# Optimization experiments

Hardware: AMD Instinct MI355X
Metric: run time of the kernel (lower is better)

## Reference

```python
import jax, jax.numpy as jnp
import numpy as np

B = 1048576  # batch size
EPS_CLAMP_LO = 1e-6
EPS_CLAMP_HI = 1.0 - 1e-6


def _build_mask():
    # mask[k, i, j] = 1 iff i + j == k, flattened to [19, 100]
    i = np.arange(10)
    m = np.zeros((19, 10, 10), dtype=np.float32)
    ii, jj = np.meshgrid(i, i, indexing='ij')
    m[(ii + jj).ravel(), ii.ravel(), jj.ravel()] = 1.0
    return jnp.asarray(m.reshape(19, 100))


def setup_inputs() -> dict:
    key = jax.random.key(0)
    k1, k2, k3, k4 = jax.random.split(key, 4)
    # concept probabilities: uniform then normalize rows to sum 1
    p1 = jax.random.uniform(k1, (B, 10), dtype=jnp.float32)
    p1 = p1 / p1.sum(axis=1, keepdims=True)
    p2 = jax.random.uniform(k2, (B, 10), dtype=jnp.float32)
    p2 = p2 / p2.sum(axis=1, keepdims=True)
    # learnable permutation-tree weights (binaryTreeLogicNet leaf maps)
    W1 = jax.random.uniform(k3, (10, 10), dtype=jnp.float32)
    W2 = jax.random.uniform(k4, (10, 10), dtype=jnp.float32)
    mask = _build_mask()
    return {"p1": p1, "p2": p2, "W1": W1, "W2": W2, "mask": mask}


def _minmax_norm(W):
    lo = W.min(axis=1, keepdims=True)
    hi = W.max(axis=1, keepdims=True)
    return (W - lo) / (hi - lo + 1e-8)


def reference(p1, p2, W1, W2, mask):
    # input_to_leaf: learned soft permutation with minmax-normalized weights
    p1p = p1 @ _minmax_norm(W1)                      # [B,10]
    p2p = p2 @ _minmax_norm(W2)                      # [B,10]
    # MinMaxAggregator graded AND at andness=1.0 -> elementwise min over all pairs
    s = jnp.minimum(p1p[:, :, None], p2p[:, None, :])  # [B,10,10]
    one_minus = 1.0 - jnp.clip(s, EPS_CLAMP_LO, EPS_CLAMP_HI)
    log_one_minus = jnp.log(one_minus + 1e-12).reshape(-1, 100)  # [B,100]
    # fused masked reduction over all 19 sum bins: [B,100] @ [100,19]
    log_prod = log_one_minus @ mask.T                # [B,19]
    y_prob = 1.0 - jnp.exp(log_prod)                 # smooth OR per sum class
    y_prob = y_prob / (y_prob.sum(axis=1, keepdims=True) + 1e-9)
    return y_prob
```

## Files before the change

### kernel.cpp

```cpp
#include <hip/hip_runtime.h>


typedef float v2f __attribute__((ext_vector_type(2)));
typedef float v4f __attribute__((ext_vector_type(4)));

#define NBLOCKS 8192
#define TPB 64
#define ROWS 2

__global__ __launch_bounds__(TPB) void bacon_main(
    const float* __restrict__ p1, const float* __restrict__ p2,
    const float* __restrict__ W1, const float* __restrict__ W2,
    float* __restrict__ out)
{
    __shared__ __align__(16) float s_out[TPB * 19];
    __shared__ __align__(16) float s_w[240];

    const int t = threadIdx.x;
    const int blk = blockIdx.x;
    const size_t base = (size_t)blk * (TPB * ROWS);

    float2 va[ROWS][5], vb[ROWS][5];
    #pragma unroll
    for (int r = 0; r < ROWS; ++r) {
        const float2* g1 = (const float2*)(p1 + (base + (size_t)r * TPB + t) * 10);
        const float2* g2 = (const float2*)(p2 + (base + (size_t)r * TPB + t) * 10);
        #pragma unroll
        for (int e = 0; e < 5; ++e) { va[r][e] = g1[e]; vb[r][e] = g2[e]; }
    }

    if (t < 20) {
        const float* row = ((t < 10) ? W1 : W2) + (t % 10) * 10;
        float r[10];
        #pragma unroll
        for (int i = 0; i < 10; ++i) r[i] = row[i];
        float lo = r[0], hi = r[0];
        #pragma unroll
        for (int i = 1; i < 10; ++i) {
            lo = fminf(lo, r[i]);
            hi = fmaxf(hi, r[i]);
        }
        float inv = 1.0f / (hi - lo + 1e-8f);
        float* o = s_w + ((t < 10) ? 0 : 120) + (t % 10) * 12;
        #pragma unroll
        for (int i = 0; i < 10; ++i) o[i] = (r[i] - lo) * inv;
        o[10] = 0.0f; o[11] = 0.0f;
    }
    __syncthreads();

    float a[ROWS][10], b[ROWS][10];
    #pragma unroll
    for (int r = 0; r < ROWS; ++r)
        #pragma unroll
        for (int e = 0; e < 5; ++e) {
            a[r][2 * e] = va[r][e].x; a[r][2 * e + 1] = va[r][e].y;
            b[r][2 * e] = vb[r][e].x; b[r][2 * e + 1] = vb[r][e].y;
        }

    v2f A2[ROWS][5], B2[ROWS][5];
    #pragma unroll
    for (int r = 0; r < ROWS; ++r)
        #pragma unroll
        for (int m = 0; m < 5; ++m) { A2[r][m] = (v2f){1.0f, 1.0f}; B2[r][m] = (v2f){1.0f, 1.0f}; }

    #pragma unroll
    for (int k = 0; k < 10; ++k) {
        const float4* w1q = (const float4*)(s_w + k * 12);
        const float4* w2q = (const float4*)(s_w + 120 + k * 12);
        float4 u0 = w1q[0], u1 = w1q[1];
        float2 u2 = *(const float2*)(s_w + k * 12 + 8);
        float4 v0 = w2q[0], v1 = w2q[1];
        float2 v2 = *(const float2*)(s_w + 120 + k * 12 + 8);
        v2f uw[5] = { {u0.x, u0.y}, {u0.z, u0.w}, {u1.x, u1.y}, {u1.z, u1.w}, {u2.x, u2.y} };
        v2f vw[5] = { {v0.x, v0.y}, {v0.z, v0.w}, {v1.x, v1.y}, {v1.z, v1.w}, {v2.x, v2.y} };
        #pragma unroll
        for (int r = 0; r < ROWS; ++r) {
            const v2f na = (v2f){-a[r][k], -a[r][k]};
            const v2f nb = (v2f){-b[r][k], -b[r][k]};
            #pragma unroll
            for (int m = 0; m < 5; ++m) {
                A2[r][m] = __builtin_elementwise_fma(na, uw[m], A2[r][m]);
                B2[r][m] = __builtin_elementwise_fma(nb, vw[m], B2[r][m]);
            }
        }
    }

    #pragma unroll
    for (int r = 0; r < ROWS; ++r) {
        float A[10], Bv[10];
        #pragma unroll
        for (int m = 0; m < 5; ++m) {
            A[2 * m] = A2[r][m].x;  A[2 * m + 1] = A2[r][m].y;
            Bv[2 * m] = B2[r][m].x; Bv[2 * m + 1] = B2[r][m].y;
        }

        float prod[19];
        #pragma unroll
        for (int k = 0; k < 19; ++k) prod[k] = 1.0f;
        #pragma unroll
        for (int i = 0; i < 10; ++i) {
            #pragma unroll
            for (int j = 0; j < 10; ++j) {
                prod[i + j] *= fmaxf(A[i], Bv[j]);
            }
        }

        float y[19];
        float tot = 0.0f;
        #pragma unroll
        for (int k = 0; k < 19; ++k) { y[k] = 1.0f - prod[k]; tot += y[k]; }
        float invn = __builtin_amdgcn_rcpf(tot + 1e-9f);

        #pragma unroll
        for (int k = 0; k < 19; ++k) s_out[t * 19 + k] = y[k] * invn;
        __syncthreads();

        {
            const v4f* so = (const v4f*)s_out;
            v4f* go = (v4f*)(out + ((size_t)blk * ROWS + r) * (TPB * 19));
            #pragma unroll
            for (int it = 0; it < 5; ++it) {
                int idx = t + it * TPB;
                if (idx < 304)
                    __builtin_nontemporal_store(so[idx], go + idx);
            }
        }
    }
}

extern "C" void kernel_launch(void* const* d_in, const int* in_sizes, int n_in,
                              void* d_out, int out_size, void* d_ws, size_t ws_size,
                              hipStream_t stream) {
    const float* p1 = (const float*)d_in[0];
    const float* p2 = (const float*)d_in[1];
    const float* W1 = (const float*)d_in[2];
    const float* W2 = (const float*)d_in[3];
    bacon_main<<<NBLOCKS, TPB, 0, stream>>>(p1, p2, W1, W2, (float*)d_out);
}
```

Measured before the change: 153.9 us.

## Make blocks persistent over panels with async triple-buffered global-to-LDS loads

Each block now handles 8 panels of 128 rows instead of 128 rows total, cutting the grid from 8192 to 1024 blocks. Inputs are fetched with global_load_lds into three LDS slots, using manual vmcnt waits so loads for later panels overlap compute on the current one. The per-row __syncthreads before the output staging is dropped, which relies on the block being a single wavefront. The goal is to hide global load latency. In exchange the kernel runs far fewer waves per CU and uses more LDS per block.

```diff
diff --git a/kernel.cpp b/kernel.cpp
--- a/kernel.cpp
+++ b/kernel.cpp
@@ -3,31 +3,43 @@
 
 typedef float v2f __attribute__((ext_vector_type(2)));
 typedef float v4f __attribute__((ext_vector_type(4)));
+typedef __attribute__((address_space(3))) unsigned int lds_u32;
+typedef const __attribute__((address_space(1))) unsigned int g_u32;
 
-#define NBLOCKS 8192
+#define NBLOCKS 1024
 #define TPB 64
-#define ROWS 2
+#define PANELS 8
+#define PROWS 128
+#define SLOTS 3
 
 __global__ __launch_bounds__(TPB) void bacon_main(
     const float* __restrict__ p1, const float* __restrict__ p2,
     const float* __restrict__ W1, const float* __restrict__ W2,
     float* __restrict__ out)
 {
+    __shared__ __align__(16) float s_in[SLOTS][2560];
     __shared__ __align__(16) float s_out[TPB * 19];
     __shared__ __align__(16) float s_w[240];
 
     const int t = threadIdx.x;
     const int blk = blockIdx.x;
-    const size_t base = (size_t)blk * (TPB * ROWS);
+    const size_t blk_row0 = (size_t)blk * (PANELS * PROWS);
 
-    float2 va[ROWS][5], vb[ROWS][5];
-    #pragma unroll
-    for (int r = 0; r < ROWS; ++r) {
-        const float2* g1 = (const float2*)(p1 + (base + (size_t)r * TPB + t) * 10);
-        const float2* g2 = (const float2*)(p2 + (base + (size_t)r * TPB + t) * 10);
+    auto stage = [&](int p, int s) {
+        g_u32* gp1 = (g_u32*)(p1 + (blk_row0 + (size_t)p * PROWS) * 10);
+        g_u32* gp2 = (g_u32*)(p2 + (blk_row0 + (size_t)p * PROWS) * 10);
+        lds_u32* l1 = (lds_u32*)&s_in[s][0];
+        lds_u32* l2 = (lds_u32*)&s_in[s][1280];
         #pragma unroll
-        for (int e = 0; e < 5; ++e) { va[r][e] = g1[e]; vb[r][e] = g2[e]; }
-    }
+        for (int i = 0; i < 5; ++i) {
+            __builtin_amdgcn_global_load_lds(gp1 + i * 256 + t * 4, l1 + i * 256, 16, 0, 0);
+            __builtin_amdgcn_global_load_lds(gp2 + i * 256 + t * 4, l2 + i * 256, 16, 0, 0);
+        }
+    };
+
+    stage(0, 0);
+    stage(1, 1);
+    stage(2, 2);
 
     if (t < 20) {
         const float* row = ((t < 10) ? W1 : W2) + (t % 10) * 10;
@@ -48,81 +60,103 @@
     }
     __syncthreads();
 
-    float a[ROWS][10], b[ROWS][10];
     #pragma unroll
-    for (int r = 0; r < ROWS; ++r)
+    for (int p = 0; p < PANELS; ++p) {
+        const int s = p % SLOTS;
+
+        if (p <= PANELS - SLOTS) {
+            asm volatile("s_waitcnt vmcnt(20)" ::: "memory");
+        } else if (p == PANELS - 2) {
+            asm volatile("s_waitcnt vmcnt(10)" ::: "memory");
+        } else {
+            asm volatile("s_waitcnt vmcnt(0)" ::: "memory");
+        }
+        __builtin_amdgcn_sched_barrier(0);
+
+        float a[2][10], b[2][10];
         #pragma unroll
-        for (int e = 0; e < 5; ++e) {
-            a[r][2 * e] = va[r][e].x; a[r][2 * e + 1] = va[r][e].y;
-            b[r][2 * e] = vb[r][e].x; b[r][2 * e + 1] = vb[r][e].y;
-        }
-
-    v2f A2[ROWS][5], B2[ROWS][5];
-    #pragma unroll
-    for (int r = 0; r < ROWS; ++r)
-        #pragma unroll
-        for (int m = 0; m < 5; ++m) { A2[r][m] = (v2f){1.0f, 1.0f}; B2[r][m] = (v2f){1.0f, 1.0f}; }
-
-    #pragma unroll
-    for (int k = 0; k < 10; ++k) {
-        const float4* w1q = (const float4*)(s_w + k * 12);
-        const float4* w2q = (const float4*)(s_w + 120 + k * 12);
-        float4 u0 = w1q[0], u1 = w1q[1];
-        float2 u2 = *(const float2*)(s_w + k * 12 + 8);
-        float4 v0 = w2q[0], v1 = w2q[1];
-        float2 v2 = *(const float2*)(s_w + 120 + k * 12 + 8);
-        v2f uw[5] = { {u0.x, u0.y}, {u0.z, u0.w}, {u1.x, u1.y}, {u1.z, u1.w}, {u2.x, u2.y} };
-        v2f vw[5] = { {v0.x, v0.y}, {v0.z, v0.w}, {v1.x, v1.y}, {v1.z, v1.w}, {v2.x, v2.y} };
-        #pragma unroll
-        for (int r = 0; r < ROWS; ++r) {
-            const v2f na = (v2f){-a[r][k], -a[r][k]};
-            const v2f nb = (v2f){-b[r][k], -b[r][k]};
+        for (int rr = 0; rr < 2; ++rr) {
+            const int row = rr * 64 + t;
+            const v2f* r1 = (const v2f*)&s_in[s][row * 10];
+            const v2f* r2 = (const v2f*)&s_in[s][1280 + row * 10];
             #pragma unroll
-            for (int m = 0; m < 5; ++m) {
-                A2[r][m] = __builtin_elementwise_fma(na, uw[m], A2[r][m]);
-                B2[r][m] = __builtin_elementwise_fma(nb, vw[m], B2[r][m]);
+            for (int e = 0; e < 5; ++e) {
+                v2f x = r1[e], y = r2[e];
+                a[rr][2 * e] = x.x; a[rr][2 * e + 1] = x.y;
+                b[rr][2 * e] = y.x; b[rr][2 * e + 1] = y.y;
             }
         }
-    }
+        asm volatile("s_waitcnt lgkmcnt(0)" ::: "memory");
+        __builtin_amdgcn_sched_barrier(0);
 
-    #pragma unroll
-    for (int r = 0; r < ROWS; ++r) {
-        float A[10], Bv[10];
+        if (p + SLOTS < PANELS) stage(p + SLOTS, s);
+
+        v2f A2[2][5], B2[2][5];
         #pragma unroll
-        for (int m = 0; m < 5; ++m) {
-            A[2 * m] = A2[r][m].x;  A[2 * m + 1] = A2[r][m].y;
-            Bv[2 * m] = B2[r][m].x; Bv[2 * m + 1] = B2[r][m].y;
-        }
+        for (int rr = 0; rr < 2; ++rr)
+            #pragma unroll
+            for (int m = 0; m < 5; ++m) { A2[rr][m] = (v2f){1.0f, 1.0f}; B2[rr][m] = (v2f){1.0f, 1.0f}; }
 
-        float prod[19];
         #pragma unroll
-        for (int k = 0; k < 19; ++k) prod[k] = 1.0f;
-        #pragma unroll
-        for (int i = 0; i < 10; ++i) {
+        for (int k = 0; k < 10; ++k) {
+            const float4* w1q = (const float4*)(s_w + k * 12);
+            const float4* w2q = (const float4*)(s_w + 120 + k * 12);
+            float4 u0 = w1q[0], u1 = w1q[1];
+            float2 u2 = *(const float2*)(s_w + k * 12 + 8);
+            float4 v0 = w2q[0], v1 = w2q[1];
+            float2 v2 = *(const float2*)(s_w + 120 + k * 12 + 8);
+            v2f uw[5] = { {u0.x, u0.y}, {u0.z, u0.w}, {u1.x, u1.y}, {u1.z, u1.w}, {u2.x, u2.y} };
+            v2f vw[5] = { {v0.x, v0.y}, {v0.z, v0.w}, {v1.x, v1.y}, {v1.z, v1.w}, {v2.x, v2.y} };
             #pragma unroll
-            for (int j = 0; j < 10; ++j) {
-                prod[i + j] *= fmaxf(A[i], Bv[j]);
+            for (int rr = 0; rr < 2; ++rr) {
+                const v2f na = (v2f){-a[rr][k], -a[rr][k]};
+                const v2f nb = (v2f){-b[rr][k], -b[rr][k]};
+                #pragma unroll
+                for (int m = 0; m < 5; ++m) {
+                    A2[rr][m] = __builtin_elementwise_fma(na, uw[m], A2[rr][m]);
+                    B2[rr][m] = __builtin_elementwise_fma(nb, vw[m], B2[rr][m]);
+                }
             }
         }
 
-        float y[19];
-        float tot = 0.0f;
         #pragma unroll
-        for (int k = 0; k < 19; ++k) { y[k] = 1.0f - prod[k]; tot += y[k]; }
-        float invn = __builtin_amdgcn_rcpf(tot + 1e-9f);
+        for (int rr = 0; rr < 2; ++rr) {
+            float A[10], Bv[10];
+            #pragma unroll
+            for (int m = 0; m < 5; ++m) {
+                A[2 * m] = A2[rr][m].x;  A[2 * m + 1] = A2[rr][m].y;
+                Bv[2 * m] = B2[rr][m].x; Bv[2 * m + 1] = B2[rr][m].y;
+            }
 
-        #pragma unroll
-        for (int k = 0; k < 19; ++k) s_out[t * 19 + k] = y[k] * invn;
-        __syncthreads();
+            float prod[19];
+            #pragma unroll
+            for (int k = 0; k < 19; ++k) prod[k] = 1.0f;
+            #pragma unroll
+            for (int i = 0; i < 10; ++i) {
+                #pragma unroll
+                for (int j = 0; j < 10; ++j) {
+                    prod[i + j] *= fmaxf(A[i], Bv[j]);
+                }
+            }
 
-        {
-            const v4f* so = (const v4f*)s_out;
-            v4f* go = (v4f*)(out + ((size_t)blk * ROWS + r) * (TPB * 19));
+            float y[19];
+            float tot = 0.0f;
             #pragma unroll
-            for (int it = 0; it < 5; ++it) {
-                int idx = t + it * TPB;
-                if (idx < 304)
-                    __builtin_nontemporal_store(so[idx], go + idx);
+            for (int k = 0; k < 19; ++k) { y[k] = 1.0f - prod[k]; tot += y[k]; }
+            float invn = __builtin_amdgcn_rcpf(tot + 1e-9f);
+
+            #pragma unroll
+            for (int k = 0; k < 19; ++k) s_out[t * 19 + k] = y[k] * invn;
+
+            {
+                const v4f* so = (const v4f*)s_out;
+                v4f* go = (v4f*)(out + (blk_row0 + (size_t)p * PROWS + rr * 64) * 19);
+                #pragma unroll
+                for (int it = 0; it < 5; ++it) {
+                    int idx = t + it * TPB;
+                    if (idx < 304)
+                        __builtin_nontemporal_store(so[idx], go + idx);
+                }
             }
         }
     }
```

Result: slower. 160.8 us (+4.5%).
